# Optimization experiments

Hardware: AMD Instinct MI355X
Metric: run time of the kernel (lower is better)

Reference implementation:

```python
import jax, jax.numpy as jnp
import numpy as np
import math

LN_EPS = 1e-5
NORM_EPS = 1e-12


def _l2norm(v):
    # F.normalize(p=2, dim=-1): v / max(||v||, eps)
    n = jnp.sqrt(jnp.sum(v * v, axis=-1, keepdims=True))
    return v / jnp.maximum(n, NORM_EPS)


def setup_inputs() -> dict:
    key = jax.random.key(0)
    B, C, P, D, R = 64, 21, 96, 256, 32
    H = D // 4  # gate MLP hidden = 64
    ks = jax.random.split(key, 24)
    f32 = jnp.float32
    inp = {
        "x": jax.random.normal(ks[0], (B * C, P, D), dtype=f32),
        "ln_w": jnp.ones((D,), f32),
        "ln_b": jnp.zeros((D,), f32),
        "Wd": jax.random.normal(ks[1], (D, R), f32) / np.sqrt(D),
        "bd": jax.random.normal(ks[2], (R,), f32) * 0.02,
        "Wq": jax.random.normal(ks[3], (R, R), f32) / np.sqrt(R),
        "Wk": jax.random.normal(ks[4], (R, R), f32) / np.sqrt(R),
        "Wv": jax.random.normal(ks[5], (R, R), f32) / np.sqrt(R),
        "Wg": jax.random.normal(ks[6], (R, R), f32) / np.sqrt(R),
        "bg": jax.random.normal(ks[7], (R,), f32) * 0.02,
        "Wu": jax.random.normal(ks[8], (R, D), f32) / np.sqrt(R),
        "bu": jax.random.normal(ks[9], (D,), f32) * 0.02,
        "cn1_w": jax.random.normal(ks[10], (1, H), f32),
        "cn1_b": jax.random.normal(ks[11], (H,), f32) * 0.02,
        "cn2_w": jax.random.normal(ks[12], (H, D), f32) / np.sqrt(H),
        "cn2_b": jnp.full((D,), -5.0, f32),
        "dn1_w": jax.random.normal(ks[13], (D, H), f32) / np.sqrt(D),
        "dn1_b": jax.random.normal(ks[14], (H,), f32) * 0.02,
        "dn2_w": jax.random.normal(ks[15], (H, D), f32) / np.sqrt(H),
        "dn2_b": jax.random.normal(ks[16], (D,), f32) * 0.02,
        "epsilon": jnp.asarray(0.1, f32),
        "B": B,
        "C": C,
    }
    return inp


def reference(x, ln_w, ln_b, Wd, bd, Wq, Wk, Wv, Wg, bg, Wu, bu,
              cn1_w, cn1_b, cn2_w, cn2_b, dn1_w, dn1_b, dn2_w, dn2_b,
              epsilon, B, C):
    BC, P, D = x.shape
    gelu = lambda t: jax.nn.gelu(t, approximate=False)

    # [B*C,P,D] -> [B*P,C,D]: mix across channels per (batch, patch)
    h = x.reshape(B, C, P, D).transpose(0, 2, 1, 3).reshape(B * P, C, D)

    # LayerNorm over D
    mu = jnp.mean(h, axis=-1, keepdims=True)
    var = jnp.var(h, axis=-1, keepdims=True)
    h_norm = (h - mu) * jax.lax.rsqrt(var + LN_EPS) * ln_w + ln_b

    # bottleneck projection down to rank
    h_low = h_norm @ Wd + bd  # [BP, C, R]

    # Hydra attention: cosine-sim linear attention, global pool over C
    Q = _l2norm(h_low @ Wq)
    K = _l2norm(h_low @ Wk)
    V = h_low @ Wv
    global_feat = jnp.sum(K * V, axis=1, keepdims=True)  # [BP, 1, R]
    h_attn = Q * global_feat  # [BP, C, R]

    # content gate in low-rank space, then project up
    gate_c = jax.nn.sigmoid(h_low @ Wg + bg)
    mixed = (h_attn * gate_c) @ Wu + bu  # [BP, C, D]

    # AdaptiveGate (hybrid): channel MLP on log C + eps * data MLP on channel variance
    log_c = math.log(max(C, 2)) / math.log(1000.0)
    lc = jnp.full((1, 1), log_c, dtype=x.dtype)
    channel_logits = gelu(lc @ cn1_w + cn1_b) @ cn2_w + cn2_b  # [1, D]
    chan_var = jnp.var(h, axis=1, ddof=1)  # unbiased var over C -> [BP, D]
    data_corr = gelu(chan_var @ dn1_w + dn1_b) @ dn2_w + dn2_b  # [BP, D]
    gate_val = jax.nn.sigmoid(channel_logits + epsilon * data_corr)[:, None, :]

    out = h + gate_val * mixed  # [BP, C, D]
    return out.reshape(B, P, C, D).transpose(0, 2, 1, 3).reshape(BC, P, D)
```

## Files before the change

kernel.cpp:

```cpp
#include <hip/hip_runtime.h>
#include <math.h>


#define DD 256
#define CC 21
#define RR 32
#define HH 64
#define PP 96
#define BB 64
#define PD (PP * DD)
#define NBP (BB * PP)
#define NT 256

#define HBS 264
#define LWS 40

#define WS_WDB  0
#define WS_W4B  16384
#define WS_WUB  24576
#define WS_DN1P 40960
#define WS_DN2P 73728
#define WS_S1   106496
#define WS_S2   106624
#define WS_LG   106752

typedef __attribute__((ext_vector_type(8))) short bf16x8;
typedef __attribute__((ext_vector_type(4))) float f32x4;
typedef __attribute__((ext_vector_type(4))) unsigned short u16x4;

__device__ __forceinline__ float gelu_exact(float x) {
    return 0.5f * x * (1.0f + erff(x * 0.70710678118654752440f));
}
__device__ __forceinline__ float sigmoidf_(float x) {
    return 1.0f / (1.0f + __expf(-x));
}
__device__ __forceinline__ short f2bf(float f) {
    union { float f; unsigned u; } v; v.f = f;
    unsigned r = v.u + 0x7FFFu + ((v.u >> 16) & 1u);
    return (short)(unsigned short)(r >> 16);
}
__device__ __forceinline__ float bf2f_s(short s) {
    union { unsigned u; float f; } v; v.u = ((unsigned)(unsigned short)s) << 16;
    return v.f;
}

#define DPP_ADD(v, ctrl)                                                      \
    (v) += __builtin_bit_cast(float, __builtin_amdgcn_update_dpp(             \
               0, __builtin_bit_cast(int, (v)), (ctrl), 0xF, 0xF, true))

__device__ __forceinline__ float rowsum16(float v) {
    DPP_ADD(v, 0xB1);
    DPP_ADD(v, 0x4E);
    DPP_ADD(v, 0x124);
    DPP_ADD(v, 0x128);
    return v;
}
__device__ __forceinline__ float rdlane(float v, int l) {
    return __builtin_bit_cast(float,
        __builtin_amdgcn_readlane(__builtin_bit_cast(int, v), l));
}

extern "C" __global__ __launch_bounds__(NT)
void hydra_preproc(const float* __restrict__ ln_w, const float* __restrict__ ln_b,
                   const float* __restrict__ Wd,   const float* __restrict__ bd,
                   const float* __restrict__ Wq,   const float* __restrict__ Wk,
                   const float* __restrict__ Wv,   const float* __restrict__ Wg,
                   const float* __restrict__ Wu,
                   const float* __restrict__ cn1w, const float* __restrict__ cn1b,
                   const float* __restrict__ cn2w, const float* __restrict__ cn2b,
                   const float* __restrict__ dn1w, const float* __restrict__ dn2w,
                   short* __restrict__ WdB, short* __restrict__ W4B,
                   short* __restrict__ WuB, short* __restrict__ dn1P,
                   short* __restrict__ dn2P,
                   float* __restrict__ s1p, float* __restrict__ s2p,
                   float* __restrict__ logits)
{
    const int t = threadIdx.x, lane = t & 63, w = t >> 6, bid = blockIdx.x;
    const int q = lane >> 4, nl = lane & 15;

    if (bid < 4) {
        int tile = bid * 4 + w;
        int kb = tile >> 1, ni = tile & 1;
        int kbase = kb * 32 + q * 8;
        int n = ni * 16 + nl;
        bf16x8 o;
        #pragma unroll
        for (int j = 0; j < 8; ++j) {
            int k = kbase + j;
            o[j] = f2bf(ln_w[k] * Wd[k * RR + n]);
        }
        *(bf16x8*)(WdB + tile * 512 + lane * 8) = o;
    } else if (bid < 6) {
        int ni = (bid - 4) * 4 + w;
        int n = ni * 16 + nl;
        const float* Wsel = (n < 32) ? Wq : (n < 64) ? Wk : (n < 96) ? Wv : Wg;
        int nn = n & 31;
        bf16x8 o;
        #pragma unroll
        for (int j = 0; j < 8; ++j) o[j] = f2bf(Wsel[(q * 8 + j) * RR + nn]);
        *(bf16x8*)(W4B + ni * 512 + lane * 8) = o;
    } else if (bid < 10) {
        int ni = (bid - 6) * 4 + w;
        int n = ni * 16 + nl;
        bf16x8 o;
        #pragma unroll
        for (int j = 0; j < 8; ++j) o[j] = f2bf(Wu[(q * 8 + j) * DD + n]);
        *(bf16x8*)(WuB + ni * 512 + lane * 8) = o;
    } else if (bid == 10) {
        __shared__ float red1[8][33], red2[8][33];
        __shared__ float clh[HH];
        int r = t & 31, ks = t >> 5;
        float a1 = 0.f, a2 = 0.f;
        for (int k = ks * 32; k < ks * 32 + 32; ++k) {
            float wv = Wd[k * RR + r];
            a1 += bf2f_s(f2bf(ln_w[k] * wv));
            a2 += ln_b[k] * wv;
        }
        red1[ks][r] = a1; red2[ks][r] = a2;
        if (t < HH) {
            const float lc = 0.44073977f;
            clh[t] = gelu_exact(lc * cn1w[t] + cn1b[t]);
        }
        __syncthreads();
        if (t < RR) {
            float s1 = 0.f, s2 = 0.f;
            #pragma unroll
            for (int s = 0; s < 8; ++s) { s1 += red1[s][t]; s2 += red2[s][t]; }
            s1p[t] = s1;
            s2p[t] = s2 + bd[t];
        }
        float a = 0.f;
        #pragma unroll 8
        for (int j = 0; j < HH; ++j) a += clh[j] * cn2w[j * DD + t];
        logits[t] = a + cn2b[t];
    } else if (bid < 19) {
        int slot = (bid - 11) * 256 + t;
        int kb = slot >> 6, j = slot & 63;
        bf16x8 o;
        #pragma unroll
        for (int ki = 0; ki < 8; ++ki) o[ki] = f2bf(dn1w[(kb * 8 + ki) * HH + j]);
        *(bf16x8*)(dn1P + slot * 8) = o;
    } else {
        int slot = (bid - 19) * 256 + t;
        int jb = slot >> 8, d = slot & 255;
        bf16x8 o;
        #pragma unroll
        for (int ji = 0; ji < 8; ++ji) o[ji] = f2bf(dn2w[(jb * 8 + ji) * DD + d]);
        *(bf16x8*)(dn2P + slot * 8) = o;
    }
}

extern "C" __global__ __launch_bounds__(NT, 8)
void hydra_fused(const float* __restrict__ x,
                 const float* __restrict__ bg,   const float* __restrict__ bu,
                 const float* __restrict__ dn1b, const float* __restrict__ dn2b,
                 const float* __restrict__ eps_p,
                 const short* __restrict__ WdB,  const short* __restrict__ W4B,
                 const short* __restrict__ WuB,  const short* __restrict__ dn1P,
                 const short* __restrict__ dn2P,
                 const float* __restrict__ s1p,  const float* __restrict__ s2p,
                 const float* __restrict__ logits,
                 float* __restrict__ out)
{
    __shared__ __align__(16) short  hbf[CC * HBS];
    __shared__ __align__(16) short  lowbf[32 * LWS];
    __shared__ __align__(16) float  sh_cv[DD];
    __shared__ __align__(16) float2 murs[32];
    __shared__ __align__(16) float  dn1p[128];
    __shared__ __align__(16) float  sh_h1[HH];
    __shared__ __align__(16) float  gfp[64];
    __shared__ __align__(16) float  sh_gf[RR];
    __shared__ __align__(16) float  sh_gate[DD];

    const int t    = threadIdx.x;
    const int lane = t & 63;
    const int w    = t >> 6;
    const int quad = lane >> 4;
    const int nl   = lane & 15;
    const int bp = blockIdx.x;
    const int b  = bp / PP;
    const int p  = bp - b * PP;
    const float* xbase = x   + (size_t)b * CC * PD + (size_t)p * DD;
    float*       obase = out + (size_t)b * CC * PD + (size_t)p * DD;

    #pragma unroll
    for (int iter = 0; iter < 6; ++iter) {
        int c = iter * 4 + w;
        bool act = (c < CC);
        float4 v = make_float4(0.f, 0.f, 0.f, 0.f);
        if (act) v = *(const float4*)(xbase + (size_t)c * PD + lane * 4);
        if (act) {
            u16x4 u;
            u[0] = (unsigned short)f2bf(v.x); u[1] = (unsigned short)f2bf(v.y);
            u[2] = (unsigned short)f2bf(v.z); u[3] = (unsigned short)f2bf(v.w);
            *(u16x4*)(hbf + c * HBS + lane * 4) = u;
        }
        float s  = v.x + v.y + v.z + v.w;
        float s2 = v.x * v.x + v.y * v.y + v.z * v.z + v.w * v.w;
        s  = rowsum16(s);
        s2 = rowsum16(s2);
        float tot  = rdlane(s, 0)  + rdlane(s, 16)  + rdlane(s, 32)  + rdlane(s, 48);
        float tot2 = rdlane(s2, 0) + rdlane(s2, 16) + rdlane(s2, 32) + rdlane(s2, 48);
        if (act && lane == 0) {
            float mu  = tot * (1.0f / DD);
            float var = tot2 * (1.0f / DD) - mu * mu;
            murs[c] = make_float2(mu, rsqrtf(var + 1e-5f));
        }
    }
    __syncthreads();

    {
        float cs = 0.f, cs2 = 0.f;
        #pragma unroll
        for (int c = 0; c < CC; ++c) {
            float v = bf2f_s(hbf[c * HBS + t]);
            cs += v; cs2 = fmaf(v, v, cs2);
        }
        sh_cv[t] = (cs2 - cs * cs * (1.0f / CC)) * (1.0f / (CC - 1));
    }
    {
        const int mt = w & 1, ct = w >> 1;
        const int c  = ct * 16 + nl;
        const int c_rd = (c < CC) ? c : (CC - 1);
        const int r0 = mt * 16 + quad * 4;
        f32x4 acc = {0.f, 0.f, 0.f, 0.f};
        #pragma unroll
        for (int kb = 0; kb < 8; ++kb) {
            bf16x8 bh = *(const bf16x8*)(hbf + c_rd * HBS + kb * 32 + quad * 8);
            bf16x8 aw = *(const bf16x8*)(WdB + (kb * 2 + mt) * 512 + lane * 8);
            acc = __builtin_amdgcn_mfma_f32_16x16x32_bf16(aw, bh, acc, 0, 0, 0);
        }
        const float2 mr = murs[c_rd];
        const f32x4 s1v = *(const f32x4*)(s1p + r0);
        const f32x4 s2v = *(const f32x4*)(s2p + r0);
        u16x4 o;
        #pragma unroll
        for (int reg = 0; reg < 4; ++reg)
            o[reg] = (unsigned short)f2bf(
                mr.y * (acc[reg] - mr.x * s1v[reg]) + s2v[reg]);
        *(u16x4*)(lowbf + c * LWS + r0) = o;
    }
    __syncthreads();

    const int mi2 = w >> 1;
    float qg0[4], qg1[4];
    if ((w & 1) == 0) {
        const int m = mi2 * 16 + nl;
        bf16x8 a = *(const bf16x8*)(lowbf + m * LWS + quad * 8);
        f32x4 acc[8];
        #pragma unroll
        for (int i = 0; i < 8; ++i) {
            bf16x8 bw = *(const bf16x8*)(W4B + i * 512 + lane * 8);
            f32x4 z = {0.f, 0.f, 0.f, 0.f};
            acc[i] = __builtin_amdgcn_mfma_f32_16x16x32_bf16(a, bw, z, 0, 0, 0);
        }
        const float bg0 = bg[nl], bg1 = bg[16 + nl];
        float kv0 = 0.f, kv1 = 0.f;
        #pragma unroll
        for (int reg = 0; reg < 4; ++reg) {
            float q0 = acc[0][reg], q1 = acc[1][reg];
            float k0 = acc[2][reg], k1 = acc[3][reg];
            float q2 = rowsum16(q0 * q0 + q1 * q1);
            float k2 = rowsum16(k0 * k0 + k1 * k1);
            float qi = 1.0f / fmaxf(sqrtf(q2), 1e-12f);
            float ki = 1.0f / fmaxf(sqrtf(k2), 1e-12f);
            float g0 = sigmoidf_(acc[6][reg] + bg0);
            float g1 = sigmoidf_(acc[7][reg] + bg1);
            qg0[reg] = q0 * qi * g0;
            qg1[reg] = q1 * qi * g1;
            int rowg = mi2 * 16 + quad * 4 + reg;
            float msk = (rowg < CC) ? 1.0f : 0.0f;
            kv0 += msk * (k0 * ki * acc[4][reg]);
            kv1 += msk * (k1 * ki * acc[5][reg]);
        }
        kv0 += __shfl_xor(kv0, 16); kv0 += __shfl_xor(kv0, 32);
        kv1 += __shfl_xor(kv1, 16); kv1 += __shfl_xor(kv1, 32);
        if (quad == 0) {
            gfp[mi2 * 32 + nl]      = kv0;
            gfp[mi2 * 32 + 16 + nl] = kv1;
        }
    } else {
        const int half = w >> 1;
        float p0 = 0.f, p1 = 0.f;
        #pragma unroll
        for (int i = 0; i < 16; ++i) {
            int kb = half * 16 + i;
            bf16x8 wv = *(const bf16x8*)(dn1P + (kb * 64 + lane) * 8);
            f32x4 c0 = *(const f32x4*)(sh_cv + kb * 8);
            f32x4 c1 = *(const f32x4*)(sh_cv + kb * 8 + 4);
            p0 += bf2f_s(wv[0]) * c0[0] + bf2f_s(wv[1]) * c0[1]
                + bf2f_s(wv[2]) * c0[2] + bf2f_s(wv[3]) * c0[3];
            p1 += bf2f_s(wv[4]) * c1[0] + bf2f_s(wv[5]) * c1[1]
                + bf2f_s(wv[6]) * c1[2] + bf2f_s(wv[7]) * c1[3];
        }
        dn1p[half * 64 + lane] = p0 + p1;
    }
    __syncthreads();

    if (t < HH) sh_h1[t] = gelu_exact(dn1p[t] + dn1p[64 + t] + dn1b[t]);
    if (t < RR) sh_gf[t] = gfp[t] + gfp[32 + t];
    __syncthreads();

    {
        const float eps = eps_p[0];
        float a0 = 0.f, a1 = 0.f;
        #pragma unroll
        for (int jb = 0; jb < 8; ++jb) {
            bf16x8 wv = *(const bf16x8*)(dn2P + (jb * 256 + t) * 8);
            f32x4 h0 = *(const f32x4*)(sh_h1 + jb * 8);
            f32x4 h1 = *(const f32x4*)(sh_h1 + jb * 8 + 4);
            a0 += bf2f_s(wv[0]) * h0[0] + bf2f_s(wv[1]) * h0[1]
                + bf2f_s(wv[2]) * h0[2] + bf2f_s(wv[3]) * h0[3];
            a1 += bf2f_s(wv[4]) * h1[0] + bf2f_s(wv[5]) * h1[1]
                + bf2f_s(wv[6]) * h1[2] + bf2f_s(wv[7]) * h1[3];
        }
        sh_gate[t] = sigmoidf_(logits[t] + eps * (a0 + a1 + dn2b[t]));
    }
    if ((w & 1) == 0) {
        float gf0 = sh_gf[nl], gf1 = sh_gf[16 + nl];
        #pragma unroll
        for (int reg = 0; reg < 4; ++reg) {
            int rowg = mi2 * 16 + quad * 4 + reg;
            lowbf[rowg * LWS + nl]      = f2bf(qg0[reg] * gf0);
            lowbf[rowg * LWS + 16 + nl] = f2bf(qg1[reg] * gf1);
        }
    }
    __syncthreads();

    {
        bf16x8 bf0 = *(const bf16x8*)(lowbf + nl * LWS + quad * 8);
        bf16x8 bf1 = *(const bf16x8*)(lowbf + (16 + nl) * LWS + quad * 8);
        const int c0 = nl, c1 = 16 + nl;
        #pragma unroll
        for (int i = 0; i < 4; ++i) {
            const int dt = w * 4 + i;
            bf16x8 af = *(const bf16x8*)(WuB + dt * 512 + lane * 8);
            f32x4 z = {0.f, 0.f, 0.f, 0.f};
            f32x4 a0 = __builtin_amdgcn_mfma_f32_16x16x32_bf16(af, bf0, z, 0, 0, 0);
            f32x4 a1 = __builtin_amdgcn_mfma_f32_16x16x32_bf16(af, bf1, z, 0, 0, 0);
            const int db = dt * 16 + quad * 4;
            const f32x4 gd  = *(const f32x4*)(sh_gate + db);
            const f32x4 bud = *(const f32x4*)(bu + db);
            {
                u16x4 h4 = *(const u16x4*)(hbf + c0 * HBS + db);
                f32x4 o;
                #pragma unroll
                for (int reg = 0; reg < 4; ++reg)
                    o[reg] = fmaf(gd[reg], a0[reg] + bud[reg],
                                  bf2f_s((short)h4[reg]));
                *(f32x4*)(obase + (size_t)c0 * PD + db) = o;
            }
            if (nl < CC - 16) {
                u16x4 h4 = *(const u16x4*)(hbf + c1 * HBS + db);
                f32x4 o;
                #pragma unroll
                for (int reg = 0; reg < 4; ++reg)
                    o[reg] = fmaf(gd[reg], a1[reg] + bud[reg],
                                  bf2f_s((short)h4[reg]));
                *(f32x4*)(obase + (size_t)c1 * PD + db) = o;
            }
        }
    }
}

extern "C" void kernel_launch(void* const* d_in, const int* in_sizes, int n_in,
                              void* d_out, int out_size, void* d_ws, size_t ws_size,
                              hipStream_t stream) {
    const float* x    = (const float*)d_in[0];
    const float* ln_w = (const float*)d_in[1];
    const float* ln_b = (const float*)d_in[2];
    const float* Wd   = (const float*)d_in[3];
    const float* bd   = (const float*)d_in[4];
    const float* Wq   = (const float*)d_in[5];
    const float* Wk   = (const float*)d_in[6];
    const float* Wv   = (const float*)d_in[7];
    const float* Wg   = (const float*)d_in[8];
    const float* bg   = (const float*)d_in[9];
    const float* Wu   = (const float*)d_in[10];
    const float* bu   = (const float*)d_in[11];
    const float* cn1w = (const float*)d_in[12];
    const float* cn1b = (const float*)d_in[13];
    const float* cn2w = (const float*)d_in[14];
    const float* cn2b = (const float*)d_in[15];
    const float* dn1w = (const float*)d_in[16];
    const float* dn1b = (const float*)d_in[17];
    const float* dn2w = (const float*)d_in[18];
    const float* dn2b = (const float*)d_in[19];
    const float* eps  = (const float*)d_in[20];
    float* out = (float*)d_out;

    char* ws = (char*)d_ws;
    short* WdB  = (short*)(ws + WS_WDB);
    short* W4B  = (short*)(ws + WS_W4B);
    short* WuB  = (short*)(ws + WS_WUB);
    short* dn1P = (short*)(ws + WS_DN1P);
    short* dn2P = (short*)(ws + WS_DN2P);
    float* s1p  = (float*)(ws + WS_S1);
    float* s2p  = (float*)(ws + WS_S2);
    float* lg   = (float*)(ws + WS_LG);

    hydra_preproc<<<27, NT, 0, stream>>>(ln_w, ln_b, Wd, bd, Wq, Wk, Wv, Wg, Wu,
                                         cn1w, cn1b, cn2w, cn2b, dn1w, dn2w,
                                         WdB, W4B, WuB, dn1P, dn2P, s1p, s2p, lg);
    hydra_fused<<<NBP, NT, 0, stream>>>(x, bg, bu, dn1b, dn2b, eps,
                                        WdB, W4B, WuB, dn1P, dn2P, s1p, s2p, lg,
                                        out);
}
```

Measured before the change: 331.7 us.

## Process two (batch,patch) rows per block to reuse weight fragments

Each block now handles two batch-patch positions, so the weight fragments for Wd, W4, Wu, dn1 and dn2 are loaded once into registers and used for both. The grid is halved and launch bounds drop to 4 waves per SIMD, and shared memory doubles. This cuts redundant global and L2 weight traffic per output. The cost is higher register and LDS use, lower occupancy and fewer blocks to hide memory latency in what is mostly a bandwidth-bound kernel.

```diff
diff --git a/kernel.cpp b/kernel.cpp
--- a/kernel.cpp
+++ b/kernel.cpp
@@ -14,6 +14,8 @@
 
 #define HBS 264
 #define LWS 40
+#define HROW (CC * HBS)
+#define LROW (32 * LWS)
 
 #define WS_WDB  0
 #define WS_W4B  16384
@@ -150,7 +152,7 @@
     }
 }
 
-extern "C" __global__ __launch_bounds__(NT, 8)
+extern "C" __global__ __launch_bounds__(NT, 4)
 void hydra_fused(const float* __restrict__ x,
                  const float* __restrict__ bg,   const float* __restrict__ bu,
                  const float* __restrict__ dn1b, const float* __restrict__ dn2b,
@@ -162,202 +164,252 @@
                  const float* __restrict__ logits,
                  float* __restrict__ out)
 {
-    __shared__ __align__(16) short  hbf[CC * HBS];
-    __shared__ __align__(16) short  lowbf[32 * LWS];
-    __shared__ __align__(16) float  sh_cv[DD];
-    __shared__ __align__(16) float2 murs[32];
-    __shared__ __align__(16) float  dn1p[128];
-    __shared__ __align__(16) float  sh_h1[HH];
-    __shared__ __align__(16) float  gfp[64];
-    __shared__ __align__(16) float  sh_gf[RR];
-    __shared__ __align__(16) float  sh_gate[DD];
+    __shared__ __align__(16) short  hbf[2 * HROW];
+    __shared__ __align__(16) short  lowbf[2 * LROW];
+    __shared__ __align__(16) float  sh_cv[2 * DD];
+    __shared__ __align__(16) float2 murs[2 * 32];
+    __shared__ __align__(16) float  dn1p[2 * 128];
+    __shared__ __align__(16) float  sh_h1[2 * HH];
+    __shared__ __align__(16) float  gfp[2 * 64];
+    __shared__ __align__(16) float  sh_gf[2 * RR];
+    __shared__ __align__(16) float  sh_gate[2 * DD];
 
     const int t    = threadIdx.x;
     const int lane = t & 63;
     const int w    = t >> 6;
     const int quad = lane >> 4;
     const int nl   = lane & 15;
-    const int bp = blockIdx.x;
-    const int b  = bp / PP;
-    const int p  = bp - b * PP;
-    const float* xbase = x   + (size_t)b * CC * PD + (size_t)p * DD;
-    float*       obase = out + (size_t)b * CC * PD + (size_t)p * DD;
-
+    const int bp0  = blockIdx.x * 2;
+
+    const float* xb[2];
+    float*       ob[2];
     #pragma unroll
-    for (int iter = 0; iter < 6; ++iter) {
-        int c = iter * 4 + w;
-        bool act = (c < CC);
-        float4 v = make_float4(0.f, 0.f, 0.f, 0.f);
-        if (act) v = *(const float4*)(xbase + (size_t)c * PD + lane * 4);
-        if (act) {
-            u16x4 u;
-            u[0] = (unsigned short)f2bf(v.x); u[1] = (unsigned short)f2bf(v.y);
-            u[2] = (unsigned short)f2bf(v.z); u[3] = (unsigned short)f2bf(v.w);
-            *(u16x4*)(hbf + c * HBS + lane * 4) = u;
-        }
-        float s  = v.x + v.y + v.z + v.w;
-        float s2 = v.x * v.x + v.y * v.y + v.z * v.z + v.w * v.w;
-        s  = rowsum16(s);
-        s2 = rowsum16(s2);
-        float tot  = rdlane(s, 0)  + rdlane(s, 16)  + rdlane(s, 32)  + rdlane(s, 48);
-        float tot2 = rdlane(s2, 0) + rdlane(s2, 16) + rdlane(s2, 32) + rdlane(s2, 48);
-        if (act && lane == 0) {
-            float mu  = tot * (1.0f / DD);
-            float var = tot2 * (1.0f / DD) - mu * mu;
-            murs[c] = make_float2(mu, rsqrtf(var + 1e-5f));
+    for (int r = 0; r < 2; ++r) {
+        int bp = bp0 + r;
+        int b  = bp / PP;
+        int p  = bp - b * PP;
+        xb[r] = x   + (size_t)b * CC * PD + (size_t)p * DD;
+        ob[r] = out + (size_t)b * CC * PD + (size_t)p * DD;
+    }
+
+    #pragma unroll
+    for (int r = 0; r < 2; ++r) {
+        #pragma unroll
+        for (int iter = 0; iter < 6; ++iter) {
+            int c = iter * 4 + w;
+            bool act = (c < CC);
+            f32x4 v = {0.f, 0.f, 0.f, 0.f};
+            if (act) v = *(const f32x4*)(xb[r] + (size_t)c * PD + lane * 4);
+            if (act) {
+                u16x4 u;
+                u[0] = (unsigned short)f2bf(v[0]); u[1] = (unsigned short)f2bf(v[1]);
+                u[2] = (unsigned short)f2bf(v[2]); u[3] = (unsigned short)f2bf(v[3]);
+                *(u16x4*)(hbf + r * HROW + c * HBS + lane * 4) = u;
+            }
+            float s  = v[0] + v[1] + v[2] + v[3];
+            float s2 = v[0]*v[0] + v[1]*v[1] + v[2]*v[2] + v[3]*v[3];
+            s  = rowsum16(s);
+            s2 = rowsum16(s2);
+            float tot  = rdlane(s, 0)  + rdlane(s, 16)  + rdlane(s, 32)  + rdlane(s, 48);
+            float tot2 = rdlane(s2, 0) + rdlane(s2, 16) + rdlane(s2, 32) + rdlane(s2, 48);
+            if (act && lane == 0) {
+                float mu  = tot * (1.0f / DD);
+                float var = tot2 * (1.0f / DD) - mu * mu;
+                murs[r * 32 + c] = make_float2(mu, rsqrtf(var + 1e-5f));
+            }
         }
     }
     __syncthreads();
 
-    {
+    #pragma unroll
+    for (int r = 0; r < 2; ++r) {
         float cs = 0.f, cs2 = 0.f;
         #pragma unroll
         for (int c = 0; c < CC; ++c) {
-            float v = bf2f_s(hbf[c * HBS + t]);
+            float v = bf2f_s(hbf[r * HROW + c * HBS + t]);
             cs += v; cs2 = fmaf(v, v, cs2);
         }
-        sh_cv[t] = (cs2 - cs * cs * (1.0f / CC)) * (1.0f / (CC - 1));
+        sh_cv[r * DD + t] = (cs2 - cs * cs * (1.0f / CC)) * (1.0f / (CC - 1));
     }
     {
         const int mt = w & 1, ct = w >> 1;
         const int c  = ct * 16 + nl;
         const int c_rd = (c < CC) ? c : (CC - 1);
         const int r0 = mt * 16 + quad * 4;
-        f32x4 acc = {0.f, 0.f, 0.f, 0.f};
-        #pragma unroll
-        for (int kb = 0; kb < 8; ++kb) {
-            bf16x8 bh = *(const bf16x8*)(hbf + c_rd * HBS + kb * 32 + quad * 8);
-            bf16x8 aw = *(const bf16x8*)(WdB + (kb * 2 + mt) * 512 + lane * 8);
-            acc = __builtin_amdgcn_mfma_f32_16x16x32_bf16(aw, bh, acc, 0, 0, 0);
-        }
-        const float2 mr = murs[c_rd];
+        bf16x8 aw[8];
+        #pragma unroll
+        for (int kb = 0; kb < 8; ++kb)
+            aw[kb] = *(const bf16x8*)(WdB + (kb * 2 + mt) * 512 + lane * 8);
         const f32x4 s1v = *(const f32x4*)(s1p + r0);
         const f32x4 s2v = *(const f32x4*)(s2p + r0);
-        u16x4 o;
-        #pragma unroll
-        for (int reg = 0; reg < 4; ++reg)
-            o[reg] = (unsigned short)f2bf(
-                mr.y * (acc[reg] - mr.x * s1v[reg]) + s2v[reg]);
-        *(u16x4*)(lowbf + c * LWS + r0) = o;
+        #pragma unroll
+        for (int r = 0; r < 2; ++r) {
+            const short* hrow = hbf + r * HROW + c_rd * HBS + quad * 8;
+            f32x4 acc = {0.f, 0.f, 0.f, 0.f};
+            #pragma unroll
+            for (int kb = 0; kb < 8; ++kb)
+                acc = __builtin_amdgcn_mfma_f32_16x16x32_bf16(
+                          aw[kb], *(const bf16x8*)(hrow + kb * 32), acc, 0, 0, 0);
+            const float2 mr = murs[r * 32 + c_rd];
+            u16x4 o;
+            #pragma unroll
+            for (int reg = 0; reg < 4; ++reg)
+                o[reg] = (unsigned short)f2bf(
+                    mr.y * (acc[reg] - mr.x * s1v[reg]) + s2v[reg]);
+            *(u16x4*)(lowbf + r * LROW + c * LWS + r0) = o;
+        }
     }
     __syncthreads();
 
     const int mi2 = w >> 1;
-    float qg0[4], qg1[4];
+    float qga[2][4], qgb[2][4];
     if ((w & 1) == 0) {
+        bf16x8 bfr[8];
+        #pragma unroll
+        for (int i = 0; i < 8; ++i)
+            bfr[i] = *(const bf16x8*)(W4B + i * 512 + lane * 8);
+        const float bg0 = bg[nl], bg1 = bg[16 + nl];
         const int m = mi2 * 16 + nl;
-        bf16x8 a = *(const bf16x8*)(lowbf + m * LWS + quad * 8);
-        f32x4 acc[8];
-        #pragma unroll
-        for (int i = 0; i < 8; ++i) {
-            bf16x8 bw = *(const bf16x8*)(W4B + i * 512 + lane * 8);
-            f32x4 z = {0.f, 0.f, 0.f, 0.f};
-            acc[i] = __builtin_amdgcn_mfma_f32_16x16x32_bf16(a, bw, z, 0, 0, 0);
-        }
-        const float bg0 = bg[nl], bg1 = bg[16 + nl];
-        float kv0 = 0.f, kv1 = 0.f;
-        #pragma unroll
-        for (int reg = 0; reg < 4; ++reg) {
-            float q0 = acc[0][reg], q1 = acc[1][reg];
-            float k0 = acc[2][reg], k1 = acc[3][reg];
-            float q2 = rowsum16(q0 * q0 + q1 * q1);
-            float k2 = rowsum16(k0 * k0 + k1 * k1);
-            float qi = 1.0f / fmaxf(sqrtf(q2), 1e-12f);
-            float ki = 1.0f / fmaxf(sqrtf(k2), 1e-12f);
-            float g0 = sigmoidf_(acc[6][reg] + bg0);
-            float g1 = sigmoidf_(acc[7][reg] + bg1);
-            qg0[reg] = q0 * qi * g0;
-            qg1[reg] = q1 * qi * g1;
-            int rowg = mi2 * 16 + quad * 4 + reg;
-            float msk = (rowg < CC) ? 1.0f : 0.0f;
-            kv0 += msk * (k0 * ki * acc[4][reg]);
-            kv1 += msk * (k1 * ki * acc[5][reg]);
-        }
-        kv0 += __shfl_xor(kv0, 16); kv0 += __shfl_xor(kv0, 32);
-        kv1 += __shfl_xor(kv1, 16); kv1 += __shfl_xor(kv1, 32);
-        if (quad == 0) {
-            gfp[mi2 * 32 + nl]      = kv0;
-            gfp[mi2 * 32 + 16 + nl] = kv1;
+        #pragma unroll
+        for (int r = 0; r < 2; ++r) {
+            bf16x8 a = *(const bf16x8*)(lowbf + r * LROW + m * LWS + quad * 8);
+            f32x4 acc[8];
+            #pragma unroll
+            for (int i = 0; i < 8; ++i) {
+                f32x4 z = {0.f, 0.f, 0.f, 0.f};
+                acc[i] = __builtin_amdgcn_mfma_f32_16x16x32_bf16(a, bfr[i], z, 0, 0, 0);
+            }
+            float kv0 = 0.f, kv1 = 0.f;
+            #pragma unroll
+            for (int reg = 0; reg < 4; ++reg) {
+                float q0 = acc[0][reg], q1 = acc[1][reg];
+                float k0 = acc[2][reg], k1 = acc[3][reg];
+                float q2 = rowsum16(q0 * q0 + q1 * q1);
+                float k2 = rowsum16(k0 * k0 + k1 * k1);
+                float qi = 1.0f / fmaxf(sqrtf(q2), 1e-12f);
+                float ki = 1.0f / fmaxf(sqrtf(k2), 1e-12f);
+                float g0 = sigmoidf_(acc[6][reg] + bg0);
+                float g1 = sigmoidf_(acc[7][reg] + bg1);
+                qga[r][reg] = q0 * qi * g0;
+                qgb[r][reg] = q1 * qi * g1;
+                int rowg = mi2 * 16 + quad * 4 + reg;
+                float msk = (rowg < CC) ? 1.0f : 0.0f;
+                kv0 += msk * (k0 * ki * acc[4][reg]);
+                kv1 += msk * (k1 * ki * acc[5][reg]);
+            }
+            kv0 += __shfl_xor(kv0, 16); kv0 += __shfl_xor(kv0, 32);
+            kv1 += __shfl_xor(kv1, 16); kv1 += __shfl_xor(kv1, 32);
+            if (quad == 0) {
+                gfp[r * 64 + mi2 * 32 + nl]      = kv0;
+                gfp[r * 64 + mi2 * 32 + 16 + nl] = kv1;
+            }
         }
     } else {
         const int half = w >> 1;
-        float p0 = 0.f, p1 = 0.f;
+        float p0a = 0.f, p1a = 0.f, p0b = 0.f, p1b = 0.f;
         #pragma unroll
         for (int i = 0; i < 16; ++i) {
             int kb = half * 16 + i;
-            bf16x8 wv = *(const bf16x8*)(dn1P + (kb * 64 + lane) * 8);
-            f32x4 c0 = *(const f32x4*)(sh_cv + kb * 8);
-            f32x4 c1 = *(const f32x4*)(sh_cv + kb * 8 + 4);
-            p0 += bf2f_s(wv[0]) * c0[0] + bf2f_s(wv[1]) * c0[1]
-                + bf2f_s(wv[2]) * c0[2] + bf2f_s(wv[3]) * c0[3];
-            p1 += bf2f_s(wv[4]) * c1[0] + bf2f_s(wv[5]) * c1[1]
-                + bf2f_s(wv[6]) * c1[2] + bf2f_s(wv[7]) * c1[3];
-        }
-        dn1p[half * 64 + lane] = p0 + p1;
+            bf16x8 wv = *(const bf16x8*)(dn1P + ((size_t)kb * 64 + lane) * 8);
+            f32x4 c0a = *(const f32x4*)(sh_cv + 0 * DD + kb * 8);
+            f32x4 c1a = *(const f32x4*)(sh_cv + 0 * DD + kb * 8 + 4);
+            f32x4 c0b = *(const f32x4*)(sh_cv + 1 * DD + kb * 8);
+            f32x4 c1b = *(const f32x4*)(sh_cv + 1 * DD + kb * 8 + 4);
+            float w0 = bf2f_s(wv[0]), w1 = bf2f_s(wv[1]), w2 = bf2f_s(wv[2]), w3 = bf2f_s(wv[3]);
+            float w4 = bf2f_s(wv[4]), w5 = bf2f_s(wv[5]), w6 = bf2f_s(wv[6]), w7 = bf2f_s(wv[7]);
+            p0a += w0 * c0a[0] + w1 * c0a[1] + w2 * c0a[2] + w3 * c0a[3];
+            p1a += w4 * c1a[0] + w5 * c1a[1] + w6 * c1a[2] + w7 * c1a[3];
+            p0b += w0 * c0b[0] + w1 * c0b[1] + w2 * c0b[2] + w3 * c0b[3];
+            p1b += w4 * c1b[0] + w5 * c1b[1] + w6 * c1b[2] + w7 * c1b[3];
+        }
+        dn1p[0 * 128 + half * 64 + lane] = p0a + p1a;
+        dn1p[1 * 128 + half * 64 + lane] = p0b + p1b;
     }
     __syncthreads();
 
-    if (t < HH) sh_h1[t] = gelu_exact(dn1p[t] + dn1p[64 + t] + dn1b[t]);
-    if (t < RR) sh_gf[t] = gfp[t] + gfp[32 + t];
+    if (t < 2 * HH) {
+        int r = t >> 6, j = t & 63;
+        sh_h1[r * HH + j] = gelu_exact(dn1p[r * 128 + j] + dn1p[r * 128 + 64 + j]
+                                       + dn1b[j]);
+    }
+    if (t < 2 * RR) {
+        int r = t >> 5, j = t & 31;
+        sh_gf[r * RR + j] = gfp[r * 64 + j] + gfp[r * 64 + 32 + j];
+    }
     __syncthreads();
 
     {
         const float eps = eps_p[0];
-        float a0 = 0.f, a1 = 0.f;
+        float a0a = 0.f, a1a = 0.f, a0b = 0.f, a1b = 0.f;
         #pragma unroll
         for (int jb = 0; jb < 8; ++jb) {
-            bf16x8 wv = *(const bf16x8*)(dn2P + (jb * 256 + t) * 8);
-            f32x4 h0 = *(const f32x4*)(sh_h1 + jb * 8);
-            f32x4 h1 = *(const f32x4*)(sh_h1 + jb * 8 + 4);
-            a0 += bf2f_s(wv[0]) * h0[0] + bf2f_s(wv[1]) * h0[1]
-                + bf2f_s(wv[2]) * h0[2] + bf2f_s(wv[3]) * h0[3];
-            a1 += bf2f_s(wv[4]) * h1[0] + bf2f_s(wv[5]) * h1[1]
-                + bf2f_s(wv[6]) * h1[2] + bf2f_s(wv[7]) * h1[3];
-        }
-        sh_gate[t] = sigmoidf_(logits[t] + eps * (a0 + a1 + dn2b[t]));
+            bf16x8 wv = *(const bf16x8*)(dn2P + ((size_t)jb * 256 + t) * 8);
+            f32x4 h0a = *(const f32x4*)(sh_h1 + 0 * HH + jb * 8);
+            f32x4 h1a = *(const f32x4*)(sh_h1 + 0 * HH + jb * 8 + 4);
+            f32x4 h0b = *(const f32x4*)(sh_h1 + 1 * HH + jb * 8);
+            f32x4 h1b = *(const f32x4*)(sh_h1 + 1 * HH + jb * 8 + 4);
+            float w0 = bf2f_s(wv[0]), w1 = bf2f_s(wv[1]), w2 = bf2f_s(wv[2]), w3 = bf2f_s(wv[3]);
+            float w4 = bf2f_s(wv[4]), w5 = bf2f_s(wv[5]), w6 = bf2f_s(wv[6]), w7 = bf2f_s(wv[7]);
+            a0a += w0 * h0a[0] + w1 * h0a[1] + w2 * h0a[2] + w3 * h0a[3];
+            a1a += w4 * h1a[0] + w5 * h1a[1] + w6 * h1a[2] + w7 * h1a[3];
+            a0b += w0 * h0b[0] + w1 * h0b[1] + w2 * h0b[2] + w3 * h0b[3];
+            a1b += w4 * h1b[0] + w5 * h1b[1] + w6 * h1b[2] + w7 * h1b[3];
+        }
+        const float lg = logits[t], db2 = dn2b[t];
+        sh_gate[0 * DD + t] = sigmoidf_(lg + eps * (a0a + a1a + db2));
+        sh_gate[1 * DD + t] = sigmoidf_(lg + eps * (a0b + a1b + db2));
     }
     if ((w & 1) == 0) {
-        float gf0 = sh_gf[nl], gf1 = sh_gf[16 + nl];
-        #pragma unroll
-        for (int reg = 0; reg < 4; ++reg) {
-            int rowg = mi2 * 16 + quad * 4 + reg;
-            lowbf[rowg * LWS + nl]      = f2bf(qg0[reg] * gf0);
-            lowbf[rowg * LWS + 16 + nl] = f2bf(qg1[reg] * gf1);
+        #pragma unroll
+        for (int r = 0; r < 2; ++r) {
+            float gf0 = sh_gf[r * RR + nl], gf1 = sh_gf[r * RR + 16 + nl];
+            #pragma unroll
+            for (int reg = 0; reg < 4; ++reg) {
+                int rowg = mi2 * 16 + quad * 4 + reg;
+                lowbf[r * LROW + rowg * LWS + nl]      = f2bf(qga[r][reg] * gf0);
+                lowbf[r * LROW + rowg * LWS + 16 + nl] = f2bf(qgb[r][reg] * gf1);
+            }
         }
     }
     __syncthreads();
 
     {
-        bf16x8 bf0 = *(const bf16x8*)(lowbf + nl * LWS + quad * 8);
-        bf16x8 bf1 = *(const bf16x8*)(lowbf + (16 + nl) * LWS + quad * 8);
+        bf16x8 af[4];
+        #pragma unroll
+        for (int i = 0; i < 4; ++i)
+            af[i] = *(const bf16x8*)(WuB + (size_t)(w * 4 + i) * 512 + lane * 8);
         const int c0 = nl, c1 = 16 + nl;
         #pragma unroll
-        for (int i = 0; i < 4; ++i) {
-            const int dt = w * 4 + i;
-            bf16x8 af = *(const bf16x8*)(WuB + dt * 512 + lane * 8);
-            f32x4 z = {0.f, 0.f, 0.f, 0.f};
-            f32x4 a0 = __builtin_amdgcn_mfma_f32_16x16x32_bf16(af, bf0, z, 0, 0, 0);
-            f32x4 a1 = __builtin_amdgcn_mfma_f32_16x16x32_bf16(af, bf1, z, 0, 0, 0);
-            const int db = dt * 16 + quad * 4;
-            const f32x4 gd  = *(const f32x4*)(sh_gate + db);
-            const f32x4 bud = *(const f32x4*)(bu + db);
-            {
-                u16x4 h4 = *(const u16x4*)(hbf + c0 * HBS + db);
-                f32x4 o;
-                #pragma unroll
-                for (int reg = 0; reg < 4; ++reg)
-                    o[reg] = fmaf(gd[reg], a0[reg] + bud[reg],
-                                  bf2f_s((short)h4[reg]));
-                *(f32x4*)(obase + (size_t)c0 * PD + db) = o;
-            }
-            if (nl < CC - 16) {
-                u16x4 h4 = *(const u16x4*)(hbf + c1 * HBS + db);
-                f32x4 o;
-                #pragma unroll
-                for (int reg = 0; reg < 4; ++reg)
-                    o[reg] = fmaf(gd[reg], a1[reg] + bud[reg],
-                                  bf2f_s((short)h4[reg]));
-                *(f32x4*)(obase + (size_t)c1 * PD + db) = o;
+        for (int r = 0; r < 2; ++r) {
+            bf16x8 bf0 = *(const bf16x8*)(lowbf + r * LROW + nl * LWS + quad * 8);
+            bf16x8 bf1 = *(const bf16x8*)(lowbf + r * LROW + (16 + nl) * LWS + quad * 8);
+            #pragma unroll
+            for (int i = 0; i < 4; ++i) {
+                const int dt = w * 4 + i;
+                f32x4 z = {0.f, 0.f, 0.f, 0.f};
+                f32x4 a0 = __builtin_amdgcn_mfma_f32_16x16x32_bf16(af[i], bf0, z, 0, 0, 0);
+                f32x4 a1 = __builtin_amdgcn_mfma_f32_16x16x32_bf16(af[i], bf1, z, 0, 0, 0);
+                const int db = dt * 16 + quad * 4;
+                const f32x4 gd  = *(const f32x4*)(sh_gate + r * DD + db);
+                const f32x4 bud = *(const f32x4*)(bu + db);
+                {
+                    u16x4 h4 = *(const u16x4*)(hbf + r * HROW + c0 * HBS + db);
+                    f32x4 o;
+                    #pragma unroll
+                    for (int reg = 0; reg < 4; ++reg)
+                        o[reg] = fmaf(gd[reg], a0[reg] + bud[reg],
+                                      bf2f_s((short)h4[reg]));
+                    *(f32x4*)(ob[r] + (size_t)c0 * PD + db) = o;
+                }
+                if (nl < CC - 16) {
+                    u16x4 h4 = *(const u16x4*)(hbf + r * HROW + c1 * HBS + db);
+                    f32x4 o;
+                    #pragma unroll
+                    for (int reg = 0; reg < 4; ++reg)
+                        o[reg] = fmaf(gd[reg], a1[reg] + bud[reg],
+                                      bf2f_s((short)h4[reg]));
+                    *(f32x4*)(ob[r] + (size_t)c1 * PD + db) = o;
+                }
             }
         }
     }
@@ -402,7 +454,7 @@
     hydra_preproc<<<27, NT, 0, stream>>>(ln_w, ln_b, Wd, bd, Wq, Wk, Wv, Wg, Wu,
                                          cn1w, cn1b, cn2w, cn2b, dn1w, dn2w,
                                          WdB, W4B, WuB, dn1P, dn2P, s1p, s2p, lg);
-    hydra_fused<<<NBP, NT, 0, stream>>>(x, bg, bu, dn1b, dn2b, eps,
-                                        WdB, W4B, WuB, dn1P, dn2P, s1p, s2p, lg,
-                                        out);
-}
+    hydra_fused<<<NBP / 2, NT, 0, stream>>>(x, bg, bu, dn1b, dn2b, eps,
+                                            WdB, W4B, WuB, dn1P, dn2P, s1p, s2p, lg,
+                                            out);
+}
```

New measurement: 316.0 us. 4.7% less time.
